# Optimization experiments

Measured on AMD Instinct MI355X. Metric: run time of the kernel, lower is better.

The kernel has to match this reference:

```python
import jax, jax.numpy as jnp
import numpy as np
from jax.scipy.special import erf

N = 4096        # n_points
M = 65536       # number of interaction events
T_MAX = 100.0   # observation window end
BETA0 = 1.0


def setup_inputs() -> dict:
    key = jax.random.key(0)
    k1, k2, k3, k4 = jax.random.split(key, 4)
    # data columns: [node_i, node_j, time] (indices stored as floats, as in the torch code)
    ij = jax.random.randint(k1, (M, 2), 0, N).astype(jnp.float32)
    times = jax.random.uniform(k2, (M,), minval=0.0, maxval=T_MAX)
    data = jnp.concatenate([ij, times[:, None]], axis=1)
    # learned parameters, initialized like the torch module
    z0 = jax.random.uniform(k3, (N, 2), dtype=jnp.float32) * 0.5
    v0 = jax.random.uniform(k4, (N, 2), dtype=jnp.float32) * 0.5
    beta = jnp.full((1, 1), BETA0, dtype=jnp.float32)
    t0 = jnp.float32(0.0)
    tn = jnp.float32(T_MAX)
    return {"data": data, "t0": t0, "tn": tn, "beta": beta, "z0": z0, "v0": v0}


def reference(data, t0, tn, beta, z0, v0):
    b = beta[0, 0]
    times = data[:, 2]                                   # (M,)
    i = jnp.floor(data[:, 0]).astype(jnp.int32)          # (M,)
    j = jnp.floor(data[:, 1]).astype(jnp.int32)          # (M,)

    # --- event term: log lambda_ij(t) = beta - ||z_i(t) - z_j(t)||^2, gathered per event.
    # (Identical to building the dense [N,N,M] tensor and fancy-indexing it.)
    zi = z0[i] + v0[i] * times[:, None]                  # (M,2)
    zj = z0[j] + v0[j] * times[:, None]                  # (M,2)
    d_event = jnp.sum((zi - zj) ** 2, axis=1)            # (M,)
    event_intensity = jnp.sum(b - d_event)

    # --- non-event term: closed-form integral of exp(beta - ||dz + dv*t||^2) over [t0, tn]
    # ||dz + dv t||^2 = a t^2 + bb t + c with a=|dv|^2, bb=2 dz.dv, c=|dz|^2
    dz = z0[:, None, :] - z0[None, :, :]                 # (N,N,2)
    dv = v0[:, None, :] - v0[None, :, :]                 # (N,N,2)
    a = jnp.sum(dv * dv, axis=-1)                        # (N,N)
    bb = 2.0 * jnp.sum(dz * dv, axis=-1)                 # (N,N)
    c = jnp.sum(dz * dz, axis=-1)                        # (N,N)
    a_safe = jnp.maximum(a, 1e-10)
    sqa = jnp.sqrt(a_safe)
    # exponent beta - (c - bb^2/(4a)) <= beta, numerically safe
    pref = (jnp.sqrt(jnp.pi) / (2.0 * sqa)) * jnp.exp(b + bb * bb / (4.0 * a_safe) - c)
    upper = erf(sqa * tn + bb / (2.0 * sqa))
    lower = erf(sqa * t0 + bb / (2.0 * sqa))
    integral = pref * (upper - lower)                    # (N,N)
    triu_mask = jnp.triu(jnp.ones((N, N), dtype=bool), k=1)
    non_event_intensity = jnp.sum(jnp.where(triu_mask, integral, 0.0))

    return event_intensity - non_event_intensity
```

## Files before the change

kernel.cpp:

```cpp
#include <hip/hip_runtime.h>


__device__ __forceinline__ float fast_erf_a(float x) {
    const float ax = __builtin_fabsf(x);
    const float t  = __builtin_amdgcn_rcpf(fmaf(0.3275911f, ax, 1.0f));
    float p = fmaf(t, 1.061405429f, -1.453152027f);
    p = fmaf(t, p, 1.421413741f);
    p = fmaf(t, p, -0.284496736f);
    p = fmaf(t, p, 0.254829592f);
    const float y = fmaf(-t * p, __expf(-ax * ax), 1.0f);
    return __builtin_copysignf(y, x);
}

__device__ __forceinline__ float fast_erf_b(float x) {
    const float ax = __builtin_fabsf(x);
    float p = fmaf(ax, 0.078108f, 0.000972f);
    p = fmaf(ax, p, 0.230389f);
    p = fmaf(ax, p, 0.278393f);
    p = fmaf(ax, p, 1.0f);
    const float w  = __builtin_amdgcn_rcpf(p);
    const float w2 = w * w;
    const float y  = fmaf(-w2, w2, 1.0f);
    return __builtin_copysignf(y, x);
}

__device__ __forceinline__ float erf_small(float x) {
    const float x2 = x * x;
    float p = fmaf(x2, 0.0052239776f, -0.0268661706f);
    p = fmaf(x2, p, 0.1128379167f);
    p = fmaf(x2, p, -0.3761263890f);
    p = fmaf(x2, p, 1.1283791671f);
    return x * p;
}

template<bool T0Z>
__device__ __forceinline__ float pair_eval(float2 zi, float2 vi,
                                           float2 zj, float2 vj,
                                           float t0, float tn, float b) {
    const float SQRT_PI_OVER_2 = 0.88622692545275801f;
    const float dzx = zi.x - zj.x, dzy = zi.y - zj.y;
    const float dvx = vi.x - vj.x, dvy = vi.y - vj.y;

    const float a  = fmaf(dvx, dvx, dvy * dvy);
    const float du = fmaf(dzx, dvx, dzy * dvy);
    const float c  = fmaf(dzx, dzx, dzy * dzy);

    const float a_safe = fmaxf(a, 1e-10f);
    const float rsq = __builtin_amdgcn_rsqf(a_safe);
    const float sqa = a_safe * rsq;
    const float u   = du * rsq;

    const float pref  = SQRT_PI_OVER_2 * rsq * __expf(fmaf(u, u, b - c));
    const float upper = fast_erf_b(fmaf(sqa, tn, u));
    const float lower = T0Z ? erf_small(u)
                            : fast_erf_a(fmaf(sqa, t0, u));
    return pref * (upper - lower);
}

__device__ __forceinline__ float block_reduce_add(float v) {
    __shared__ float smem[16];
    #pragma unroll
    for (int off = 32; off > 0; off >>= 1)
        v += __shfl_down(v, off, 64);
    const int lane = threadIdx.x & 63;
    const int wave = threadIdx.x >> 6;
    if (lane == 0) smem[wave] = v;
    __syncthreads();
    if (threadIdx.x == 0) {
        float s = smem[0];
        const int nw = (int)blockDim.x >> 6;
        for (int w = 1; w < nw; ++w) s += smem[w];
        return s;
    }
    return 0.0f;
}

template<bool T0Z>
__device__ __forceinline__ float pair_tile(int q, int jofs, int N,
                                           const float2* __restrict__ z2,
                                           const float2* __restrict__ v2,
                                           float t0, float tn, float b) {
    const int i0 = 2 * q,      i1 = i0 + 1;
    const int i2 = N - 2 - i0, i3 = i2 + 1;
    const bool g1 = (i1 < N);
    const bool g2 = (i2 > i1);
    const bool g3 = (i3 > i1) && (i3 < N);

    float a0 = 0.0f, a1 = 0.0f, a2 = 0.0f, a3 = 0.0f;

    const float2 zi0 = z2[i0], vi0 = v2[i0];
    const float2 zi1 = g1 ? z2[i1] : zi0, vi1 = g1 ? v2[i1] : vi0;
    #pragma unroll 2
    for (int j = i0 + 1 + jofs; j < N; j += 512) {
        const float2 zj = z2[j], vj = v2[j];
        a0 += pair_eval<T0Z>(zi0, vi0, zj, vj, t0, tn, b);
        const float e1 = pair_eval<T0Z>(zi1, vi1, zj, vj, t0, tn, b);
        a1 += (g1 && j > i1) ? e1 : 0.0f;
    }

    if (g2) {
        const float2 zi2 = z2[i2], vi2 = v2[i2];
        const float2 zi3 = g3 ? z2[i3] : zi2, vi3 = g3 ? v2[i3] : vi2;
        #pragma unroll 2
        for (int j = i2 + 1 + jofs; j < N; j += 512) {
            const float2 zj = z2[j], vj = v2[j];
            a2 += pair_eval<T0Z>(zi2, vi2, zj, vj, t0, tn, b);
            const float e3 = pair_eval<T0Z>(zi3, vi3, zj, vj, t0, tn, b);
            a3 += (g3 && j > i3) ? e3 : 0.0f;
        }
    }
    return (a0 + a1) + (a2 + a3);
}

__global__ void __launch_bounds__(256)
fused_kernel(const float* __restrict__ data,
             const float* __restrict__ t0p,
             const float* __restrict__ tnp,
             const float* __restrict__ beta,
             const float* __restrict__ z0,
             const float* __restrict__ v0,
             float* __restrict__ ws, int M, int N) {
    const float t0 = t0p[0];
    const float tn = tnp[0];
    const float b  = beta[0];
    const float2* __restrict__ z2 = (const float2*)z0;
    const float2* __restrict__ v2 = (const float2*)v0;

    const int q    = (int)blockIdx.x >> 1;
    const int jofs = (((int)blockIdx.x & 1) << 8) + (int)threadIdx.x;

    float acc;
    if (t0 == 0.0f)
        acc = -pair_tile<true >(q, jofs, N, z2, v2, t0, tn, b);
    else
        acc = -pair_tile<false>(q, jofs, N, z2, v2, t0, tn, b);

    const int chunk = (M + (int)gridDim.x - 1) / (int)gridDim.x;
    const int mbeg  = (int)blockIdx.x * chunk;
    const int mend  = min(mbeg + chunk, M);
    for (int m = mbeg + (int)threadIdx.x; m < mend; m += 256) {
        const float fi = data[3 * m + 0];
        const float fj = data[3 * m + 1];
        const float t  = data[3 * m + 2];
        const int ii = (int)fi;
        const int jj = (int)fj;
        const float2 zi = z2[ii], zj = z2[jj];
        const float2 vi = v2[ii], vj = v2[jj];
        const float dx = (zi.x - zj.x) + (vi.x - vj.x) * t;
        const float dy = (zi.y - zj.y) + (vi.y - vj.y) * t;
        acc += b - (dx * dx + dy * dy);
    }

    const float s = block_reduce_add(acc);
    if (threadIdx.x == 0) ws[blockIdx.x] = s;
}

__global__ void __launch_bounds__(1024)
finalize_kernel(const float* __restrict__ ws, float* __restrict__ out,
                int nblocks) {
    const float4* __restrict__ ws4 = (const float4*)ws;
    const int n4 = nblocks >> 2;
    float v = 0.0f;
    for (int k = threadIdx.x; k < n4; k += 1024) {
        const float4 p = ws4[k];
        v += (p.x + p.y) + (p.z + p.w);
    }
    if (threadIdx.x == 0)
        for (int k = n4 << 2; k < nblocks; ++k) v += ws[k];
    const float s = block_reduce_add(v);
    if (threadIdx.x == 0) out[0] = s;
}

extern "C" void kernel_launch(void* const* d_in, const int* in_sizes, int n_in,
                              void* d_out, int out_size, void* d_ws, size_t ws_size,
                              hipStream_t stream) {
    const float* data = (const float*)d_in[0];
    const float* t0   = (const float*)d_in[1];
    const float* tn   = (const float*)d_in[2];
    const float* beta = (const float*)d_in[3];
    const float* z0   = (const float*)d_in[4];
    const float* v0   = (const float*)d_in[5];
    float* out = (float*)d_out;
    float* ws  = (float*)d_ws;

    const int M = in_sizes[0] / 3;
    const int N = in_sizes[4] / 2;

    const int ntiles = (N + 3) / 4;
    const int blocks = 2 * ntiles;
    fused_kernel<<<blocks, 256, 0, stream>>>(data, t0, tn, beta, z0, v0, ws, M, N);
    finalize_kernel<<<1, 1024, 0, stream>>>(ws, out, blocks);
}
```

Baseline: 77.40 us.

## Evaluate four rows per j-load in quad tiles and fold exp(beta) into constant

Each tile now covers four consecutive rows at the low end and four at the high end, so each loaded j column is reused for four pair evaluations instead of two. Blocks per tile grow from two to four with a 1024 column stride, which keeps the grid at 2048 blocks. The exp(beta) factor is hoisted into a per-block constant Kb, which removes one add from the exponent per pair. The row masking switches to clamped indices with a sentinel compare, so more lanes do masked, wasted work near the diagonal.

```diff
diff --git a/kernel.cpp b/kernel.cpp
--- a/kernel.cpp
+++ b/kernel.cpp
@@ -36,8 +36,7 @@
 template<bool T0Z>
 __device__ __forceinline__ float pair_eval(float2 zi, float2 vi,
                                            float2 zj, float2 vj,
-                                           float t0, float tn, float b) {
-    const float SQRT_PI_OVER_2 = 0.88622692545275801f;
+                                           float t0, float tn, float Kb) {
     const float dzx = zi.x - zj.x, dzy = zi.y - zj.y;
     const float dvx = vi.x - vj.x, dvy = vi.y - vj.y;
 
@@ -50,7 +49,7 @@
     const float sqa = a_safe * rsq;
     const float u   = du * rsq;
 
-    const float pref  = SQRT_PI_OVER_2 * rsq * __expf(fmaf(u, u, b - c));
+    const float pref  = Kb * rsq * __expf(fmaf(u, u, -c));
     const float upper = fast_erf_b(fmaf(sqa, tn, u));
     const float lower = T0Z ? erf_small(u)
                             : fast_erf_a(fmaf(sqa, t0, u));
@@ -76,40 +75,39 @@
 }
 
 template<bool T0Z>
-__device__ __forceinline__ float pair_tile(int q, int jofs, int N,
+__device__ __forceinline__ float quad_tile(int r0, int rvalid_lo, int jofs, int N,
                                            const float2* __restrict__ z2,
                                            const float2* __restrict__ v2,
-                                           float t0, float tn, float b) {
-    const int i0 = 2 * q,      i1 = i0 + 1;
-    const int i2 = N - 2 - i0, i3 = i2 + 1;
-    const bool g1 = (i1 < N);
-    const bool g2 = (i2 > i1);
-    const bool g3 = (i3 > i1) && (i3 < N);
-
-    float a0 = 0.0f, a1 = 0.0f, a2 = 0.0f, a3 = 0.0f;
-
-    const float2 zi0 = z2[i0], vi0 = v2[i0];
-    const float2 zi1 = g1 ? z2[i1] : zi0, vi1 = g1 ? v2[i1] : vi0;
-    #pragma unroll 2
-    for (int j = i0 + 1 + jofs; j < N; j += 512) {
+                                           float t0, float tn, float Kb) {
+    const int r1 = r0 + 1, r2i = r0 + 2, r3 = r0 + 3;
+    const int hi = N - 1;
+    const int c0 = min(max(r0, 0), hi), c1 = min(max(r1, 0), hi);
+    const int c2 = min(max(r2i, 0), hi), c3 = min(max(r3, 0), hi);
+
+    const float2 zr0 = z2[c0], vr0 = v2[c0];
+    const float2 zr1 = z2[c1], vr1 = v2[c1];
+    const float2 zr2 = z2[c2], vr2 = v2[c2];
+    const float2 zr3 = z2[c3], vr3 = v2[c3];
+
+    const int BIG = 0x7fffffff;
+    const int m0 = (r0  >= rvalid_lo && r0  < N) ? r0  : BIG;
+    const int m1 = (r1  >= rvalid_lo && r1  < N) ? r1  : BIG;
+    const int m2 = (r2i >= rvalid_lo && r2i < N) ? r2i : BIG;
+    const int m3 = (r3  >= rvalid_lo && r3  < N) ? r3  : BIG;
+
+    float s0 = 0.0f, s1 = 0.0f, s2 = 0.0f, s3 = 0.0f;
+    for (int j = r0 + 1 + jofs; j < N; j += 1024) {
         const float2 zj = z2[j], vj = v2[j];
-        a0 += pair_eval<T0Z>(zi0, vi0, zj, vj, t0, tn, b);
-        const float e1 = pair_eval<T0Z>(zi1, vi1, zj, vj, t0, tn, b);
-        a1 += (g1 && j > i1) ? e1 : 0.0f;
-    }
-
-    if (g2) {
-        const float2 zi2 = z2[i2], vi2 = v2[i2];
-        const float2 zi3 = g3 ? z2[i3] : zi2, vi3 = g3 ? v2[i3] : vi2;
-        #pragma unroll 2
-        for (int j = i2 + 1 + jofs; j < N; j += 512) {
-            const float2 zj = z2[j], vj = v2[j];
-            a2 += pair_eval<T0Z>(zi2, vi2, zj, vj, t0, tn, b);
-            const float e3 = pair_eval<T0Z>(zi3, vi3, zj, vj, t0, tn, b);
-            a3 += (g3 && j > i3) ? e3 : 0.0f;
-        }
-    }
-    return (a0 + a1) + (a2 + a3);
+        const float e0 = pair_eval<T0Z>(zr0, vr0, zj, vj, t0, tn, Kb);
+        const float e1 = pair_eval<T0Z>(zr1, vr1, zj, vj, t0, tn, Kb);
+        const float e2 = pair_eval<T0Z>(zr2, vr2, zj, vj, t0, tn, Kb);
+        const float e3 = pair_eval<T0Z>(zr3, vr3, zj, vj, t0, tn, Kb);
+        s0 += (j > m0) ? e0 : 0.0f;
+        s1 += (j > m1) ? e1 : 0.0f;
+        s2 += (j > m2) ? e2 : 0.0f;
+        s3 += (j > m3) ? e3 : 0.0f;
+    }
+    return (s0 + s1) + (s2 + s3);
 }
 
 __global__ void __launch_bounds__(256)
@@ -123,17 +121,26 @@
     const float t0 = t0p[0];
     const float tn = tnp[0];
     const float b  = beta[0];
+    const float Kb = 0.88622692545275801f * __expf(b);
     const float2* __restrict__ z2 = (const float2*)z0;
     const float2* __restrict__ v2 = (const float2*)v0;
 
-    const int q    = (int)blockIdx.x >> 1;
-    const int jofs = (((int)blockIdx.x & 1) << 8) + (int)threadIdx.x;
-
+    const int ntiles  = (N + 7) / 8;
+    const int q       = (int)blockIdx.x >> 2;
+    const int jofs    = (((int)blockIdx.x & 3) << 8) + (int)threadIdx.x;
+    const int rlow    = 4 * q;
+    const int rhigh   = N - 4 - rlow;
+    const int hilimit = 4 * ntiles;
     float acc;
-    if (t0 == 0.0f)
-        acc = -pair_tile<true >(q, jofs, N, z2, v2, t0, tn, b);
-    else
-        acc = -pair_tile<false>(q, jofs, N, z2, v2, t0, tn, b);
+    if (t0 == 0.0f) {
+        float s = quad_tile<true >(rlow,  0,       jofs, N, z2, v2, t0, tn, Kb);
+        s      += quad_tile<true >(rhigh, hilimit, jofs, N, z2, v2, t0, tn, Kb);
+        acc = -s;
+    } else {
+        float s = quad_tile<false>(rlow,  0,       jofs, N, z2, v2, t0, tn, Kb);
+        s      += quad_tile<false>(rhigh, hilimit, jofs, N, z2, v2, t0, tn, Kb);
+        acc = -s;
+    }
 
     const int chunk = (M + (int)gridDim.x - 1) / (int)gridDim.x;
     const int mbeg  = (int)blockIdx.x * chunk;
@@ -186,8 +193,8 @@
     const int M = in_sizes[0] / 3;
     const int N = in_sizes[4] / 2;
 
-    const int ntiles = (N + 3) / 4;
-    const int blocks = 2 * ntiles;
+    const int ntiles = (N + 7) / 8;
+    const int blocks = 4 * ntiles;
     fused_kernel<<<blocks, 256, 0, stream>>>(data, t0, tn, beta, z0, v0, ws, M, N);
     finalize_kernel<<<1, 1024, 0, stream>>>(ws, out, blocks);
 }
```

After: 77.17 us. No clear change (-0.3%).
